# Performance work log

Hardware: AMD Instinct MI355X
Metric: run time of the kernel (lower is better)

The kernel has to match this reference:

```python
import jax, jax.numpy as jnp
import numpy as np
from jax import lax

D_STATE, D_ADAPT, D_CNN, D_RNN, D_OUT, HORIZON = 12, 16, 64, 256, 2, 10
B, L, H, W = 32, 16, 112, 112
DN = ('NCHW', 'OIHW', 'NCHW')
BN_EPS = 1e-5


def setup_inputs() -> dict:
    key = jax.random.key(0)
    ks = jax.random.split(key, 22)
    rn = lambda k, shape, s=0.05: jax.random.normal(k, shape, jnp.float32) * s
    return {
        'x': jax.random.normal(ks[0], (B, L, D_STATE), jnp.float32),
        'frames': jax.random.normal(ks[1], (B, L, 3, H, W), jnp.float32),
        # backbone `cnn`: 16x16 stride-16 patchify conv 3 -> 576 (gives 7x7 spatial)
        'cnn_w': rn(ks[2], (576, 3, 16, 16)), 'cnn_b': rn(ks[3], (576,)),
        # cnn_1: Conv2d(576, 64, 3, padding=1) + ReLU + BatchNorm (eval) + Dropout (eval=identity)
        'cnn1_w': rn(ks[4], (D_CNN, 576, 3, 3)), 'cnn1_b': rn(ks[5], (D_CNN,)),
        'bn_g': jnp.ones((D_CNN,), jnp.float32), 'bn_b': jnp.zeros((D_CNN,), jnp.float32),
        'bn_m': jnp.zeros((D_CNN,), jnp.float32), 'bn_v': jnp.ones((D_CNN,), jnp.float32),
        'a0_w': rn(ks[6], (D_ADAPT, D_STATE)), 'a0_b': rn(ks[7], (D_ADAPT,)),
        'ai_w': rn(ks[8], (D_ADAPT, D_ADAPT)), 'ai_b': rn(ks[9], (D_ADAPT,)),
        'an_w': rn(ks[10], (D_RNN, D_CNN + D_ADAPT)), 'an_b': rn(ks[11], (D_RNN,)),
        # single-layer batch_first GRU, PyTorch gate layout [r, z, n]
        'w_ih': rn(ks[12], (3 * D_RNN, D_RNN)), 'w_hh': rn(ks[13], (3 * D_RNN, D_RNN)),
        'b_ih': rn(ks[14], (3 * D_RNN,)), 'b_hh': rn(ks[15], (3 * D_RNN,)),
        'fi_w': rn(ks[16], (D_RNN, D_RNN)), 'fi_b': rn(ks[17], (D_RNN,)),
        'fn_w': rn(ks[18], (D_OUT, D_RNN)), 'fn_b': rn(ks[19], (D_OUT,)),
    }


def _gru_cell(xt, h, w_ih, w_hh, b_ih, b_hh):
    gi = xt @ w_ih.T + b_ih  # (B, 3*D)
    gh = h @ w_hh.T + b_hh
    i_r, i_z, i_n = jnp.split(gi, 3, axis=-1)
    h_r, h_z, h_n = jnp.split(gh, 3, axis=-1)
    r = jax.nn.sigmoid(i_r + h_r)
    z = jax.nn.sigmoid(i_z + h_z)
    n = jnp.tanh(i_n + r * h_n)
    return (1.0 - z) * n + z * h


def _forward(x, frames, cnn_w, cnn_b, cnn1_w, cnn1_b, bn_g, bn_b, bn_m, bn_v,
             a0_w, a0_b, ai_w, ai_b, an_w, an_b, w_ih, w_hh, b_ih, b_hh,
             fi_w, fi_b, fn_w, fn_b):
    b, l = frames.shape[0], frames.shape[1]
    f = frames.reshape((-1,) + frames.shape[-3:])  # (b*l, 3, H, W)
    # backbone cnn: patchify conv -> (b*l, 576, 7, 7)
    f = lax.conv_general_dilated(f, cnn_w, (16, 16), 'VALID', dimension_numbers=DN) + cnn_b[:, None, None]
    # cnn_1: Conv3x3 same -> ReLU -> BatchNorm(eval) -> Dropout(eval=identity)
    f = lax.conv_general_dilated(f, cnn1_w, (1, 1), 'SAME', dimension_numbers=DN) + cnn1_b[:, None, None]
    f = jax.nn.relu(f)
    inv = bn_g / jnp.sqrt(bn_v + BN_EPS)
    f = (f - bn_m[:, None, None]) * inv[:, None, None] + bn_b[:, None, None]
    # AdaptiveAvgPool2d((1,1)) then reshape to (b, l, d_cnn)
    f = f.mean(axis=(2, 3)).reshape(b, l, -1)
    # state adapters
    s = jax.nn.relu(x @ a0_w.T + a0_b)
    s = s + jax.nn.relu(s @ ai_w.T + ai_b)
    s = jnp.concatenate([s, f], axis=-1)  # (b, l, d_cnn + d_adapt)
    s = jax.nn.relu(s @ an_w.T + an_b)    # (b, l, d_rnn)
    # encoder GRU over the l frames
    d_rnn = w_hh.shape[1]
    h0 = jnp.zeros((b, d_rnn), s.dtype)
    def enc_step(h, xt):
        h2 = _gru_cell(xt, h, w_ih, w_hh, b_ih, b_hh)
        return h2, None
    h, _ = lax.scan(enc_step, h0, jnp.swapaxes(s, 0, 1))
    x_in = h  # last output of single-layer GRU == final hidden state
    def dec_step(carry, _):
        xi, hh = carry
        hn = _gru_cell(xi, hh, w_ih, w_hh, b_ih, b_hh)  # one GRU step; output == new hidden
        xr = hn + jax.nn.relu(hn @ fi_w.T + fi_b)       # final_i residual
        pred = jnp.tanh(xr @ fn_w.T + fn_b)             # final_n head
        return (xr, hn), pred
    _, preds = lax.scan(dec_step, (x_in, h), None, length=HORIZON)
    return preds[:, :, None, :]  # (horizon, b, 1, d_out) matching torch.stack of (b,1,d_out)


def reference(x, frames, cnn_w, cnn_b, cnn1_w, cnn1_b, bn_g, bn_b, bn_m, bn_v,
              a0_w, a0_b, ai_w, ai_b, an_w, an_b, w_ih, w_hh, b_ih, b_hh,
              fi_w, fi_b, fn_w, fn_b):
    return _forward(x, frames, cnn_w, cnn_b, cnn1_w, cnn1_b, bn_g, bn_b, bn_m, bn_v,
                    a0_w, a0_b, ai_w, ai_b, an_w, an_b, w_ih, w_hh, b_ih, b_hh,
                    fi_w, fi_b, fn_w, fn_b)
```

## Files before the change

### kernel.cpp

```cpp
#include <hip/hip_runtime.h>

typedef unsigned short u16;
typedef unsigned int u32;
typedef __bf16 bf16x8 __attribute__((ext_vector_type(8)));
typedef float f32x4 __attribute__((ext_vector_type(4)));
typedef unsigned short u16x8 __attribute__((ext_vector_type(8)));
typedef unsigned int u32x4 __attribute__((ext_vector_type(4)));
typedef _Float16 v2h __attribute__((ext_vector_type(2)));

__device__ __forceinline__ u16 f2bf(float f) {
    unsigned u = __float_as_uint(f);
    u = (u + 0x7fffu + ((u >> 16) & 1u)) >> 16;
    return (u16)u;
}
__device__ __forceinline__ float bf2f(u16 h) {
    return __uint_as_float((unsigned)h << 16);
}
__device__ __forceinline__ u32 packh2(float a, float b) {
    _Float16 ha = (_Float16)a, hb = (_Float16)b;
    u16 la = __builtin_bit_cast(u16, ha), lb = __builtin_bit_cast(u16, hb);
    return (u32)la | ((u32)lb << 16);
}
__device__ __forceinline__ float dot2acc(u32 w, u32 h, float acc) {
#if __has_builtin(__builtin_amdgcn_fdot2)
    return __builtin_amdgcn_fdot2(__builtin_bit_cast(v2h, w),
                                  __builtin_bit_cast(v2h, h), acc, false);
#else
    v2h wv = __builtin_bit_cast(v2h, w), hv = __builtin_bit_cast(v2h, h);
    return acc + (float)wv.x * (float)hv.x + (float)wv.y * (float)hv.y;
#endif
}
__device__ __forceinline__ float dot8(u32x4 w, u32x4 h, float acc) {
    acc = dot2acc(w.x, h.x, acc);
    acc = dot2acc(w.y, h.y, acc);
    acc = dot2acc(w.z, h.z, acc);
    acc = dot2acc(w.w, h.w, acc);
    return acc;
}
__device__ __forceinline__ void gload_lds16(const void* g, void* l) {
    __builtin_amdgcn_global_load_lds(
        (const __attribute__((address_space(1))) unsigned int*)g,
        (__attribute__((address_space(3))) unsigned int*)l, 16, 0, 0);
}
__device__ __forceinline__ void barrier_lds() {
    __builtin_amdgcn_s_waitcnt(0xC07F);
    __builtin_amdgcn_s_barrier();
}

__global__ __launch_bounds__(256) void prep_kernel(
    const float* __restrict__ cnn_w, const float* __restrict__ cnn1_w,
    const float* __restrict__ w_hh, const float* __restrict__ w_ih,
    const float* __restrict__ fi_w, const float* __restrict__ frames,
    u16* __restrict__ B1, u16* __restrict__ B2,
    u32* __restrict__ whh8, u32* __restrict__ wih8, u32* __restrict__ fi8,
    u32* __restrict__ zpage, u16* __restrict__ fbf)
{
    if (blockIdx.x >= 3924) {
        size_t i = ((size_t)(blockIdx.x - 3924) * 256 + threadIdx.x) * 8;
        float4 a = *(const float4*)(frames + i);
        float4 b = *(const float4*)(frames + i + 4);
        u16x8 v = { f2bf(a.x), f2bf(a.y), f2bf(a.z), f2bf(a.w),
                    f2bf(b.x), f2bf(b.y), f2bf(b.z), f2bf(b.w) };
        __builtin_nontemporal_store(v, (u16x8*)(fbf + i));
        return;
    }
    int idx = blockIdx.x * 256 + threadIdx.x;
    if (idx < 442368) { B1[idx] = f2bf(cnn_w[idx]); return; }
    idx -= 442368;
    if (idx < 331776) {
        int n = idx / 5184, rem = idx - n * 5184;
        int off = rem / 576, c = rem - off * 576;
        int dy = off / 3, dx = off - dy * 3;
        B2[idx] = f2bf(cnn1_w[((n * 576 + c) * 3 + dy) * 3 + dx]);
        return;
    }
    idx -= 331776;
    if (idx < 98304) {
        int kb = idx / 3072, r = idx - kb * 3072;
        int o = r >> 2, c = r & 3;
        int kk = kb * 8 + c * 2;
        whh8[idx] = packh2(w_hh[o * 256 + kk], w_hh[o * 256 + kk + 1]);
        return;
    }
    idx -= 98304;
    if (idx < 98304) {
        int kb = idx / 3072, r = idx - kb * 3072;
        int o = r >> 2, c = r & 3;
        int kk = kb * 8 + c * 2;
        wih8[idx] = packh2(w_ih[o * 256 + kk], w_ih[o * 256 + kk + 1]);
        return;
    }
    idx -= 98304;
    if (idx < 32768) {
        int kb = idx / 1024, r = idx - kb * 1024;
        int u = r >> 2, c = r & 3;
        int kk = kb * 8 + c * 2;
        fi8[idx] = packh2(fi_w[u * 256 + kk], fi_w[u * 256 + kk + 1]);
        return;
    }
    idx -= 32768;
    if (idx < 1024) zpage[idx] = 0u;
}

__global__ __launch_bounds__(256) void gemm1_v2(
    const u16* __restrict__ fbf, const u16* __restrict__ B1,
    const float* __restrict__ cnn_b, u16* __restrict__ f1)
{
    __shared__ u16 As[128 * 64];
    __shared__ u16 Bs[64 * 64];
    const int t = threadIdx.x, bx = blockIdx.x;
    const int m0 = (bx / 9) * 128, n0 = (bx % 9) * 64;
    const int wave = t >> 6, lane = t & 63;
    const int lm = lane & 15, lq = lane >> 4;

    f32x4 acc[2][4];
#pragma unroll
    for (int i = 0; i < 2; ++i)
#pragma unroll
        for (int q = 0; q < 4; ++q) acc[i][q] = (f32x4){0.f, 0.f, 0.f, 0.f};

    int ac8[4]; size_t abase[4];
#pragma unroll
    for (int i = 0; i < 4; ++i) {
        int s = wave * 256 + i * 64 + lane;
        int row = s >> 3, cc = s & 7;
        ac8[i] = cc ^ (row & 7);
        int m = m0 + row;
        int fr = m / 49, pos = m - fr * 49;
        int py = pos / 7, px = pos - py * 7;
        abase[i] = (size_t)fr * 37632 + py * 1792 + px * 16;
    }
    int bn[2], bc8[2];
#pragma unroll
    for (int i = 0; i < 2; ++i) {
        int s = wave * 128 + i * 64 + lane;
        int n = s >> 3, cc = s & 7;
        bn[i] = n; bc8[i] = cc ^ (n & 7);
    }

    for (int kt = 0; kt < 12; ++kt) {
        const int k0 = kt * 64;
#pragma unroll
        for (int i = 0; i < 4; ++i) {
            int k = k0 + ac8[i] * 8;
            int c = k >> 8, dy = (k >> 4) & 15, dx = k & 15;
            gload_lds16(fbf + abase[i] + c * 12544 + dy * 112 + dx,
                        &As[(wave * 256 + i * 64) * 8]);
        }
#pragma unroll
        for (int i = 0; i < 2; ++i) {
            gload_lds16(B1 + (size_t)(n0 + bn[i]) * 768 + k0 + bc8[i] * 8,
                        &Bs[(wave * 128 + i * 64) * 8]);
        }
        __syncthreads();
#pragma unroll
        for (int s = 0; s < 2; ++s) {
            bf16x8 a[2], b[4];
#pragma unroll
            for (int mi = 0; mi < 2; ++mi) {
                int row = wave * 32 + mi * 16 + lm;
                int c8 = s * 4 + lq;
                a[mi] = *(const bf16x8*)(&As[(row * 8 + (c8 ^ (row & 7))) * 8]);
            }
#pragma unroll
            for (int q = 0; q < 4; ++q) {
                int n = q * 16 + lm;
                int c8 = s * 4 + lq;
                b[q] = *(const bf16x8*)(&Bs[(n * 8 + (c8 ^ (n & 7))) * 8]);
            }
#pragma unroll
            for (int mi = 0; mi < 2; ++mi)
#pragma unroll
                for (int q = 0; q < 4; ++q)
                    acc[mi][q] = __builtin_amdgcn_mfma_f32_16x16x32_bf16(a[mi], b[q], acc[mi][q], 0, 0, 0);
        }
        __syncthreads();
    }
#pragma unroll
    for (int mi = 0; mi < 2; ++mi) {
#pragma unroll
        for (int q = 0; q < 4; ++q) {
            int n = n0 + q * 16 + lm;
            float bias = cnn_b[n];
#pragma unroll
            for (int r = 0; r < 4; ++r) {
                int m = m0 + wave * 32 + mi * 16 + lq * 4 + r;
                __builtin_nontemporal_store(f2bf(acc[mi][q][r] + bias), &f1[(size_t)m * 576 + n]);
            }
        }
    }
}

__global__ __launch_bounds__(256) void gemm1_patchify(
    const float* __restrict__ frames, const u16* __restrict__ B1,
    const float* __restrict__ cnn_b, u16* __restrict__ f1)
{
    __shared__ u16 As[128 * 64];
    __shared__ u16 Bs[64 * 64];
    const int t = threadIdx.x;
    const int bx = blockIdx.x;
    const int m0 = (bx / 9) * 128;
    const int n0 = (bx % 9) * 64;
    const int wave = t >> 6, lane = t & 63;
    const int lm = lane & 15, lq = lane >> 4;

    f32x4 acc[2][4];
#pragma unroll
    for (int i = 0; i < 2; ++i)
#pragma unroll
        for (int q = 0; q < 4; ++q) acc[i][q] = (f32x4){0.f, 0.f, 0.f, 0.f};

    int arow[4], ac8[4], abase[4];
#pragma unroll
    for (int i = 0; i < 4; ++i) {
        int cid = t + i * 256;
        int row = cid >> 3, c8 = cid & 7;
        int m = m0 + row;
        int fr = m / 49, pos = m - fr * 49;
        int py = pos / 7, px = pos - py * 7;
        arow[i] = row; ac8[i] = c8;
        abase[i] = (fr * 3 * 112 + py * 16) * 112 + px * 16;
    }

    for (int kt = 0; kt < 12; ++kt) {
        const int k0 = kt * 64;
#pragma unroll
        for (int i = 0; i < 4; ++i) {
            int k = k0 + ac8[i] * 8;
            int c = k >> 8, dy = (k >> 4) & 15, dx = k & 15;
            const float* src = frames + abase[i] + (c * 112 + dy) * 112 + dx;
            float4 v0 = *(const float4*)src;
            float4 v1 = *(const float4*)(src + 4);
            u16x8 v = { f2bf(v0.x), f2bf(v0.y), f2bf(v0.z), f2bf(v0.w),
                        f2bf(v1.x), f2bf(v1.y), f2bf(v1.z), f2bf(v1.w) };
            int sidx = arow[i] * 8 + (ac8[i] ^ (arow[i] & 7));
            *(u16x8*)(&As[sidx * 8]) = v;
        }
#pragma unroll
        for (int i = 0; i < 2; ++i) {
            int cid = t + i * 256;
            int n = cid >> 3, c8 = cid & 7;
            u16x8 v = *(const u16x8*)(B1 + (size_t)(n0 + n) * 768 + k0 + c8 * 8);
            int sidx = n * 8 + (c8 ^ (n & 7));
            *(u16x8*)(&Bs[sidx * 8]) = v;
        }
        __syncthreads();
#pragma unroll
        for (int s = 0; s < 2; ++s) {
            bf16x8 a[2], b[4];
#pragma unroll
            for (int mi = 0; mi < 2; ++mi) {
                int row = wave * 32 + mi * 16 + lm;
                int c8 = s * 4 + lq;
                a[mi] = *(const bf16x8*)(&As[(row * 8 + (c8 ^ (row & 7))) * 8]);
            }
#pragma unroll
            for (int q = 0; q < 4; ++q) {
                int n = q * 16 + lm;
                int c8 = s * 4 + lq;
                b[q] = *(const bf16x8*)(&Bs[(n * 8 + (c8 ^ (n & 7))) * 8]);
            }
#pragma unroll
            for (int mi = 0; mi < 2; ++mi)
#pragma unroll
                for (int q = 0; q < 4; ++q)
                    acc[mi][q] = __builtin_amdgcn_mfma_f32_16x16x32_bf16(a[mi], b[q], acc[mi][q], 0, 0, 0);
        }
        __syncthreads();
    }
#pragma unroll
    for (int mi = 0; mi < 2; ++mi) {
#pragma unroll
        for (int q = 0; q < 4; ++q) {
            int n = n0 + q * 16 + lm;
            float bias = cnn_b[n];
#pragma unroll
            for (int r = 0; r < 4; ++r) {
                int m = m0 + wave * 32 + mi * 16 + lq * 4 + r;
                __builtin_nontemporal_store(f2bf(acc[mi][q][r] + bias), &f1[(size_t)m * 576 + n]);
            }
        }
    }
}

__global__ __launch_bounds__(256) void gemm2_v2(
    const u16* __restrict__ f1, const u16* __restrict__ B2,
    const u16* __restrict__ zpage, float* __restrict__ C2)
{
    __shared__ u16 As[64 * 64];
    __shared__ u16 Bs[64 * 64];
    const int t = threadIdx.x;
    const int m0 = blockIdx.x * 64;
    const int wave = t >> 6, lane = t & 63;
    const int lm = lane & 15, lq = lane >> 4;

    f32x4 acc[4];
#pragma unroll
    for (int q = 0; q < 4; ++q) acc[q] = (f32x4){0.f, 0.f, 0.f, 0.f};

    int ac8[2], afr[2], apy[2], apx[2];
#pragma unroll
    for (int i = 0; i < 2; ++i) {
        int s = wave * 128 + i * 64 + lane;
        int row = s >> 3, cc = s & 7;
        ac8[i] = cc ^ (row & 7);
        int m = m0 + row;
        int fr = m / 49, pos = m - fr * 49;
        int py = pos / 7;
        afr[i] = fr; apy[i] = py; apx[i] = pos - py * 7;
    }
    int bn[2], bc8[2];
#pragma unroll
    for (int i = 0; i < 2; ++i) {
        int s = wave * 128 + i * 64 + lane;
        int n = s >> 3, cc = s & 7;
        bn[i] = n; bc8[i] = cc ^ (n & 7);
    }

    for (int kt = 0; kt < 81; ++kt) {
        int off = kt / 9, cb = kt - off * 9;
        int dy = off / 3, dx = off - dy * 3;
        int c0 = cb * 64;
#pragma unroll
        for (int i = 0; i < 2; ++i) {
            int yy = apy[i] + dy - 1, xx = apx[i] + dx - 1;
            const u16* g = ((unsigned)yy < 7u && (unsigned)xx < 7u)
                ? f1 + ((size_t)(afr[i] * 49 + yy * 7 + xx)) * 576 + c0 + ac8[i] * 8
                : zpage;
            gload_lds16(g, &As[(wave * 128 + i * 64) * 8]);
        }
#pragma unroll
        for (int i = 0; i < 2; ++i) {
            gload_lds16(B2 + (size_t)bn[i] * 5184 + kt * 64 + bc8[i] * 8,
                        &Bs[(wave * 128 + i * 64) * 8]);
        }
        __syncthreads();
#pragma unroll
        for (int s = 0; s < 2; ++s) {
            int row = wave * 16 + lm;
            int c8 = s * 4 + lq;
            bf16x8 a = *(const bf16x8*)(&As[(row * 8 + (c8 ^ (row & 7))) * 8]);
            bf16x8 b[4];
#pragma unroll
            for (int q = 0; q < 4; ++q) {
                int n = q * 16 + lm;
                b[q] = *(const bf16x8*)(&Bs[(n * 8 + (c8 ^ (n & 7))) * 8]);
            }
#pragma unroll
            for (int q = 0; q < 4; ++q)
                acc[q] = __builtin_amdgcn_mfma_f32_16x16x32_bf16(a, b[q], acc[q], 0, 0, 0);
        }
        __syncthreads();
    }
#pragma unroll
    for (int q = 0; q < 4; ++q)
#pragma unroll
        for (int r = 0; r < 4; ++r) {
            int m = m0 + wave * 16 + lq * 4 + r;
            int n = q * 16 + lm;
            __builtin_nontemporal_store(acc[q][r], &C2[(size_t)m * 64 + n]);
        }
}

__global__ __launch_bounds__(256) void reduce_kernel(
    const float* __restrict__ C2, const float* __restrict__ cnn1_b,
    const float* __restrict__ bn_g, const float* __restrict__ bn_b,
    const float* __restrict__ bn_m, const float* __restrict__ bn_v,
    float* __restrict__ fmean)
{
    int idx = blockIdx.x * 256 + threadIdx.x;
    int bl = idx >> 6, ch = idx & 63;
    float bias = cnn1_b[ch];
    const float* p = C2 + (size_t)bl * 49 * 64 + ch;
    float s = 0.f;
#pragma unroll
    for (int i = 0; i < 49; ++i) s += fmaxf(p[i * 64] + bias, 0.f);
    float mean = s * (1.f / 49.f);
    float inv = bn_g[ch] * rsqrtf(bn_v[ch] + 1e-5f);
    fmean[idx] = (mean - bn_m[ch]) * inv + bn_b[ch];
}

__global__ __launch_bounds__(256) void adapt_prep2_kernel(
    const float* __restrict__ x, const float* __restrict__ fmean,
    const float* __restrict__ a0_w, const float* __restrict__ a0_b,
    const float* __restrict__ ai_w, const float* __restrict__ ai_b,
    const float* __restrict__ an_w, const float* __restrict__ an_b,
    const float* __restrict__ w_ih,
    u16* __restrict__ zx_hi, u16* __restrict__ zx_lo,
    u16* __restrict__ wih_hi, u16* __restrict__ wih_lo)
{
    const int t = threadIdx.x;
    if (blockIdx.x >= 512) {
        int idx = (blockIdx.x - 512) * 256 + t;
        float v = w_ih[idx];
        u16 hi = f2bf(v);
        wih_hi[idx] = hi;
        wih_lo[idx] = f2bf(v - bf2f(hi));
        return;
    }
    const int bl = blockIdx.x;
    __shared__ float s0[16];
    __shared__ float sf[80];
    if (t < 16) {
        float a = a0_b[t];
        const float* xp = x + bl * 12;
#pragma unroll
        for (int i = 0; i < 12; ++i) a += xp[i] * a0_w[t * 12 + i];
        s0[t] = fmaxf(a, 0.f);
    }
    __syncthreads();
    if (t < 16) {
        float a = ai_b[t];
#pragma unroll
        for (int i = 0; i < 16; ++i) a += s0[i] * ai_w[t * 16 + i];
        sf[t] = s0[t] + fmaxf(a, 0.f);
    } else if (t < 80) {
        sf[t] = fmean[bl * 64 + (t - 16)];
    }
    __syncthreads();
    float a = an_b[t];
#pragma unroll 8
    for (int i = 0; i < 80; ++i) a += sf[i] * an_w[t * 80 + i];
    a = fmaxf(a, 0.f);
    u16 hi = f2bf(a);
    zx_hi[bl * 256 + t] = hi;
    zx_lo[bl * 256 + t] = f2bf(a - bf2f(hi));
}

__global__ __launch_bounds__(256) void gi_kernel(
    const u16* __restrict__ zx_hi, const u16* __restrict__ zx_lo,
    const u16* __restrict__ wih_hi, const u16* __restrict__ wih_lo,
    const float* __restrict__ b_ih, float* __restrict__ gi_pre)
{
    __shared__ u16 Ah[128 * 64], Al[128 * 64];
    __shared__ u16 Bh[64 * 64], Bl[64 * 64];
    const int t = threadIdx.x, bx = blockIdx.x;
    const int m0 = (bx / 12) * 128, n0 = (bx % 12) * 64;
    const int wave = t >> 6, lane = t & 63;
    const int lm = lane & 15, lq = lane >> 4;

    f32x4 acc[2][4];
#pragma unroll
    for (int i = 0; i < 2; ++i)
#pragma unroll
        for (int q = 0; q < 4; ++q) acc[i][q] = (f32x4){0.f, 0.f, 0.f, 0.f};

    for (int kt = 0; kt < 4; ++kt) {
        const int k0 = kt * 64;
#pragma unroll
        for (int i = 0; i < 4; ++i) {
            int cid = t + i * 256;
            int row = cid >> 3, c8 = cid & 7;
            size_t src = (size_t)(m0 + row) * 256 + k0 + c8 * 8;
            int sidx = (row * 8 + (c8 ^ (row & 7))) * 8;
            *(u16x8*)(&Ah[sidx]) = *(const u16x8*)(zx_hi + src);
            *(u16x8*)(&Al[sidx]) = *(const u16x8*)(zx_lo + src);
        }
#pragma unroll
        for (int i = 0; i < 2; ++i) {
            int cid = t + i * 256;
            int n = cid >> 3, c8 = cid & 7;
            size_t src = (size_t)(n0 + n) * 256 + k0 + c8 * 8;
            int sidx = (n * 8 + (c8 ^ (n & 7))) * 8;
            *(u16x8*)(&Bh[sidx]) = *(const u16x8*)(wih_hi + src);
            *(u16x8*)(&Bl[sidx]) = *(const u16x8*)(wih_lo + src);
        }
        __syncthreads();
#pragma unroll
        for (int s = 0; s < 2; ++s) {
            bf16x8 ah[2], al[2], bh[4], blv[4];
#pragma unroll
            for (int mi = 0; mi < 2; ++mi) {
                int row = wave * 32 + mi * 16 + lm;
                int c8 = s * 4 + lq;
                int sidx = (row * 8 + (c8 ^ (row & 7))) * 8;
                ah[mi] = *(const bf16x8*)(&Ah[sidx]);
                al[mi] = *(const bf16x8*)(&Al[sidx]);
            }
#pragma unroll
            for (int q = 0; q < 4; ++q) {
                int n = q * 16 + lm;
                int c8 = s * 4 + lq;
                int sidx = (n * 8 + (c8 ^ (n & 7))) * 8;
                bh[q] = *(const bf16x8*)(&Bh[sidx]);
                blv[q] = *(const bf16x8*)(&Bl[sidx]);
            }
#pragma unroll
            for (int mi = 0; mi < 2; ++mi)
#pragma unroll
                for (int q = 0; q < 4; ++q) {
                    acc[mi][q] = __builtin_amdgcn_mfma_f32_16x16x32_bf16(ah[mi], bh[q], acc[mi][q], 0, 0, 0);
                    acc[mi][q] = __builtin_amdgcn_mfma_f32_16x16x32_bf16(ah[mi], blv[q], acc[mi][q], 0, 0, 0);
                    acc[mi][q] = __builtin_amdgcn_mfma_f32_16x16x32_bf16(al[mi], bh[q], acc[mi][q], 0, 0, 0);
                }
        }
        __syncthreads();
    }
#pragma unroll
    for (int q = 0; q < 4; ++q) {
        int n = n0 + q * 16 + lm;
        float bias = b_ih[n];
#pragma unroll
        for (int mi = 0; mi < 2; ++mi)
#pragma unroll
            for (int r = 0; r < 4; ++r) {
                int m = m0 + wave * 32 + mi * 16 + lq * 4 + r;
                gi_pre[(size_t)m * 768 + n] = acc[mi][q][r] + bias;
            }
    }
}

__global__ __launch_bounds__(768) void rnn_stream5(
    const float* __restrict__ gi_pre,
    const u32x4* __restrict__ whh8, const u32x4* __restrict__ wih8,
    const u32x4* __restrict__ fi8,
    const float* __restrict__ b_ih, const float* __restrict__ b_hh,
    const float* __restrict__ fi_b,
    const float* __restrict__ fn_w, const float* __restrict__ fn_b,
    float* __restrict__ out)
{
    extern __shared__ __align__(16) u32 slab[];
    const int b = blockIdx.x, t = threadIdx.x;
    const int wave = t >> 6;
    __shared__ __align__(16) u32 h2[128];
    __shared__ __align__(16) u32 x2[128];
    __shared__ float sA[768];
    __shared__ float sB[256];
    __shared__ float parts[768];
    __shared__ float pp[8];

#pragma unroll
    for (int j = 0; j < 12; ++j)
        *(u32x4*)&slab[(j * 768 + t) * 4] = whh8[j * 768 + t];

    u32x4 whr[20];
#pragma unroll
    for (int j = 0; j < 20; ++j) whr[j] = whh8[(size_t)(12 + j) * 768 + t];

    const float bhh = b_hh[t];
    const float bih = b_ih[t];
    float hprev = 0.f;
    if (t < 128) h2[t] = 0u;
    __syncthreads();

    for (int l = 0; l < 16; ++l) {
        float gi = gi_pre[(size_t)(b * 16 + l) * 768 + t];
        float a0 = 0.f, a1 = 0.f;
#pragma unroll
        for (int j = 0; j < 12; ++j) {
            u32x4 ws = *(const u32x4*)&slab[(j * 768 + t) * 4];
            u32x4 hh = *(const u32x4*)&h2[j * 4];
            if (j & 1) a1 = dot8(ws, hh, a1); else a0 = dot8(ws, hh, a0);
        }
#pragma unroll
        for (int j = 0; j < 20; ++j) {
            u32x4 hh = *(const u32x4*)&h2[(12 + j) * 4];
            if (j & 1) a1 = dot8(whr[j], hh, a1); else a0 = dot8(whr[j], hh, a0);
        }
        float ah = a0 + a1;
        if (t < 512) sA[t] = gi + ah + bhh;
        else { sA[t] = gi; sB[t - 512] = ah + bhh; }
        barrier_lds();
        if (t < 256) {
            float r = 1.f / (1.f + expf(-sA[t]));
            float z = 1.f / (1.f + expf(-sA[256 + t]));
            float n = tanhf(sA[512 + t] + r * sB[t]);
            hprev = (1.f - z) * n + z * hprev;
            float partner = __shfl_xor(hprev, 1);
            if ((t & 1) == 0) h2[t >> 1] = packh2(hprev, partner);
        }
        barrier_lds();
    }

    float xprev = hprev;
    if (t < 128) x2[t] = h2[t];
    __syncthreads();
    const int u_ = t & 255, s_ = t >> 8;

    for (int d = 0; d < 10; ++d) {
        float a0 = 0.f, a1 = 0.f, x0 = 0.f, x1 = 0.f;
#pragma unroll 4
        for (int j = 0; j < 32; ++j) {
            int jj = (j + wave * 3) & 31;
            u32x4 w = wih8[(size_t)jj * 768 + t];
            u32x4 xx = *(const u32x4*)&x2[jj * 4];
            if (j & 1) x1 = dot8(w, xx, x1); else x0 = dot8(w, xx, x0);
        }
#pragma unroll
        for (int j = 0; j < 12; ++j) {
            u32x4 ws = *(const u32x4*)&slab[(j * 768 + t) * 4];
            u32x4 hh = *(const u32x4*)&h2[j * 4];
            if (j & 1) a1 = dot8(ws, hh, a1); else a0 = dot8(ws, hh, a0);
        }
#pragma unroll
        for (int j = 0; j < 20; ++j) {
            u32x4 hh = *(const u32x4*)&h2[(12 + j) * 4];
            if (j & 1) a1 = dot8(whr[j], hh, a1); else a0 = dot8(whr[j], hh, a0);
        }
        float ah = a0 + a1, ax = x0 + x1;
        if (t < 512) sA[t] = ax + bih + ah + bhh;
        else { sA[t] = ax + bih; sB[t - 512] = ah + bhh; }
        barrier_lds();
        u32x4 fw[11];
        int cnt = 0;
#pragma unroll
        for (int j = 0; j < 11; ++j) {
            int jj = s_ + j * 3;
            if (jj < 32) { fw[j] = fi8[jj * 256 + u_]; cnt = j + 1; }
        }
        if (t < 256) {
            float r = 1.f / (1.f + expf(-sA[t]));
            float z = 1.f / (1.f + expf(-sA[256 + t]));
            float n = tanhf(sA[512 + t] + r * sB[t]);
            hprev = (1.f - z) * n + z * hprev;
            float partner = __shfl_xor(hprev, 1);
            if ((t & 1) == 0) h2[t >> 1] = packh2(hprev, partner);
        }
        barrier_lds();
        {
            float f0 = 0.f, f1v = 0.f;
#pragma unroll
            for (int j = 0; j < 11; ++j) {
                if (j < cnt) {
                    int jj = s_ + j * 3;
                    u32x4 hh = *(const u32x4*)&h2[jj * 4];
                    if (j & 1) f1v = dot8(fw[j], hh, f1v); else f0 = dot8(fw[j], hh, f0);
                }
            }
            parts[t] = f0 + f1v;
        }
        barrier_lds();
        if (t < 256) {
            float a = parts[t] + parts[256 + t] + parts[512 + t] + fi_b[t];
            xprev = hprev + fmaxf(a, 0.f);
            float partner = __shfl_xor(xprev, 1);
            if ((t & 1) == 0) x2[t >> 1] = packh2(xprev, partner);
            float c0 = xprev * fn_w[t];
            float c1 = xprev * fn_w[256 + t];
#pragma unroll
            for (int off = 32; off >= 1; off >>= 1) {
                c0 += __shfl_down(c0, off);
                c1 += __shfl_down(c1, off);
            }
            if ((t & 63) == 0) { pp[(t >> 6) * 2] = c0; pp[(t >> 6) * 2 + 1] = c1; }
        }
        barrier_lds();
        if (t < 2)
            out[d * 64 + b * 2 + t] =
                tanhf(fn_b[t] + pp[t] + pp[2 + t] + pp[4 + t] + pp[6 + t]);
    }
}

extern "C" void kernel_launch(void* const* d_in, const int* in_sizes, int n_in,
                              void* d_out, int out_size, void* d_ws, size_t ws_size,
                              hipStream_t stream)
{
    const float* x      = (const float*)d_in[0];
    const float* frames = (const float*)d_in[1];
    const float* cnn_w  = (const float*)d_in[2];
    const float* cnn_b  = (const float*)d_in[3];
    const float* cnn1_w = (const float*)d_in[4];
    const float* cnn1_b = (const float*)d_in[5];
    const float* bn_g   = (const float*)d_in[6];
    const float* bn_b   = (const float*)d_in[7];
    const float* bn_m   = (const float*)d_in[8];
    const float* bn_v   = (const float*)d_in[9];
    const float* a0_w   = (const float*)d_in[10];
    const float* a0_b   = (const float*)d_in[11];
    const float* ai_w   = (const float*)d_in[12];
    const float* ai_b   = (const float*)d_in[13];
    const float* an_w   = (const float*)d_in[14];
    const float* an_b   = (const float*)d_in[15];
    const float* w_ih   = (const float*)d_in[16];
    const float* w_hh   = (const float*)d_in[17];
    const float* b_ih   = (const float*)d_in[18];
    const float* b_hh   = (const float*)d_in[19];
    const float* fi_w   = (const float*)d_in[20];
    const float* fi_b   = (const float*)d_in[21];
    const float* fn_w   = (const float*)d_in[22];
    const float* fn_b   = (const float*)d_in[23];
    float* out = (float*)d_out;

    char* ws = (char*)d_ws;
    u16*   f1     = (u16*)(ws);
    u16*   B1     = (u16*)(ws + 28901376);
    u16*   B2     = (u16*)(ws + 29786112);
    float* C2     = (float*)(ws + 30449664);
    float* fmean  = (float*)(ws + 36872192);
    u32*   whh8   = (u32*)(ws + 37003264);
    u32*   wih8   = (u32*)(ws + 37396480);
    u32*   fi8    = (u32*)(ws + 37789696);
    u32*   zpage  = (u32*)(ws + 37920768);
    float* gi_pre = (float*)(ws + 30449664);
    u16*   wih_hi = (u16*)(ws + 32022528);
    u16*   wih_lo = (u16*)(ws + 32415744);
    u16*   zx_hi  = (u16*)(ws + 32808960);
    u16*   zx_lo  = (u16*)(ws + 33071104);
    u16*   fbf    = (u16*)(ws + 37924864);

    const bool big = ws_size >= 76460032ull;

    prep_kernel<<<big ? 13332 : 3924, 256, 0, stream>>>(
        cnn_w, cnn1_w, w_hh, w_ih, fi_w, frames,
        B1, B2, whh8, wih8, fi8, zpage, fbf);
    if (big) {
        gemm1_v2<<<196 * 9, 256, 0, stream>>>(fbf, B1, cnn_b, f1);
    } else {
        gemm1_patchify<<<196 * 9, 256, 0, stream>>>(frames, B1, cnn_b, f1);
    }
    gemm2_v2<<<392, 256, 0, stream>>>(f1, B2, (const u16*)zpage, C2);
    reduce_kernel<<<128, 256, 0, stream>>>(C2, cnn1_b, bn_g, bn_b, bn_m, bn_v, fmean);
    adapt_prep2_kernel<<<1280, 256, 0, stream>>>(x, fmean, a0_w, a0_b, ai_w, ai_b,
                                                 an_w, an_b, w_ih,
                                                 zx_hi, zx_lo, wih_hi, wih_lo);
    gi_kernel<<<48, 256, 0, stream>>>(zx_hi, zx_lo, wih_hi, wih_lo, b_ih, gi_pre);
    hipFuncSetAttribute((const void*)rnn_stream5,
                        hipFuncAttributeMaxDynamicSharedMemorySize, 147456);
    rnn_stream5<<<32, 768, 147456, stream>>>(gi_pre, (const u32x4*)whh8,
                                             (const u32x4*)wih8, (const u32x4*)fi8,
                                             b_ih, b_hh, fi_b, fn_w, fn_b, out);
}
```

Measured before the change: 422.7 us.

## Triple-buffer conv GEMM with larger M tile, stream GRU weights, fast activations

The 3x3 conv GEMM now uses 128-row tiles with a three-stage LDS ring. Async global-to-LDS loads for tile kt+2 are issued while tile kt is computed, with one barrier per step, which should hide load latency and reuse the B tile across more rows. The GRU kernel stops holding 20 w_hh blocks in registers and streams them from global/L2 each step with a staggered start per wave, freeing registers at the cost of repeated weight reads. Sigmoid and tanh switch to __expf-based formulas, which are cheaper but less precise.

```diff
diff --git a/kernel.cpp b/kernel.cpp
--- a/kernel.cpp
+++ b/kernel.cpp
@@ -46,6 +46,8 @@
     __builtin_amdgcn_s_waitcnt(0xC07F);
     __builtin_amdgcn_s_barrier();
 }
+__device__ __forceinline__ float fsig(float x) { return 1.f / (1.f + __expf(-x)); }
+__device__ __forceinline__ float ftanh(float x) { return 1.f - 2.f / (1.f + __expf(2.f * x)); }
 
 __global__ __launch_bounds__(256) void prep_kernel(
     const float* __restrict__ cnn_w, const float* __restrict__ cnn1_w,
@@ -283,25 +285,27 @@
     }
 }
 
-__global__ __launch_bounds__(256) void gemm2_v2(
+__global__ __launch_bounds__(256) void gemm2_v3(
     const u16* __restrict__ f1, const u16* __restrict__ B2,
     const u16* __restrict__ zpage, float* __restrict__ C2)
 {
-    __shared__ u16 As[64 * 64];
-    __shared__ u16 Bs[64 * 64];
+    __shared__ u16 As[3][128 * 64];
+    __shared__ u16 Bs[3][64 * 64];
     const int t = threadIdx.x;
-    const int m0 = blockIdx.x * 64;
+    const int m0 = blockIdx.x * 128;
     const int wave = t >> 6, lane = t & 63;
     const int lm = lane & 15, lq = lane >> 4;
 
-    f32x4 acc[4];
-#pragma unroll
-    for (int q = 0; q < 4; ++q) acc[q] = (f32x4){0.f, 0.f, 0.f, 0.f};
-
-    int ac8[2], afr[2], apy[2], apx[2];
-#pragma unroll
-    for (int i = 0; i < 2; ++i) {
-        int s = wave * 128 + i * 64 + lane;
+    f32x4 acc[2][4];
+#pragma unroll
+    for (int i = 0; i < 2; ++i)
+#pragma unroll
+        for (int q = 0; q < 4; ++q) acc[i][q] = (f32x4){0.f, 0.f, 0.f, 0.f};
+
+    int ac8[4], afr[4], apy[4], apx[4];
+#pragma unroll
+    for (int i = 0; i < 4; ++i) {
+        int s = wave * 256 + i * 64 + lane;
         int row = s >> 3, cc = s & 7;
         ac8[i] = cc ^ (row & 7);
         int m = m0 + row;
@@ -317,49 +321,68 @@
         bn[i] = n; bc8[i] = cc ^ (n & 7);
     }
 
-    for (int kt = 0; kt < 81; ++kt) {
+    auto issue = [&](int kt, int buf) {
         int off = kt / 9, cb = kt - off * 9;
         int dy = off / 3, dx = off - dy * 3;
         int c0 = cb * 64;
 #pragma unroll
-        for (int i = 0; i < 2; ++i) {
+        for (int i = 0; i < 4; ++i) {
             int yy = apy[i] + dy - 1, xx = apx[i] + dx - 1;
             const u16* g = ((unsigned)yy < 7u && (unsigned)xx < 7u)
                 ? f1 + ((size_t)(afr[i] * 49 + yy * 7 + xx)) * 576 + c0 + ac8[i] * 8
                 : zpage;
-            gload_lds16(g, &As[(wave * 128 + i * 64) * 8]);
+            gload_lds16(g, &As[buf][(wave * 256 + i * 64) * 8]);
         }
 #pragma unroll
         for (int i = 0; i < 2; ++i) {
             gload_lds16(B2 + (size_t)bn[i] * 5184 + kt * 64 + bc8[i] * 8,
-                        &Bs[(wave * 128 + i * 64) * 8]);
-        }
-        __syncthreads();
+                        &Bs[buf][(wave * 128 + i * 64) * 8]);
+        }
+    };
+
+    issue(0, 0);
+    issue(1, 1);
+
+    for (int kt = 0; kt < 81; ++kt) {
+        const int cur = kt % 3;
+        if (kt < 80) __builtin_amdgcn_s_waitcnt(0x0F76);
+        else         __builtin_amdgcn_s_waitcnt(0x0F70);
+        __builtin_amdgcn_s_barrier();
+        __asm__ volatile("" ::: "memory");
+        if (kt + 2 <= 80) issue(kt + 2, (kt + 2) % 3);
 #pragma unroll
         for (int s = 0; s < 2; ++s) {
-            int row = wave * 16 + lm;
-            int c8 = s * 4 + lq;
-            bf16x8 a = *(const bf16x8*)(&As[(row * 8 + (c8 ^ (row & 7))) * 8]);
-            bf16x8 b[4];
+            bf16x8 a[2], b[4];
+#pragma unroll
+            for (int mi = 0; mi < 2; ++mi) {
+                int row = wave * 32 + mi * 16 + lm;
+                int c8 = s * 4 + lq;
+                a[mi] = *(const bf16x8*)(&As[cur][(row * 8 + (c8 ^ (row & 7))) * 8]);
+            }
 #pragma unroll
             for (int q = 0; q < 4; ++q) {
                 int n = q * 16 + lm;
-                b[q] = *(const bf16x8*)(&Bs[(n * 8 + (c8 ^ (n & 7))) * 8]);
-            }
-#pragma unroll
-            for (int q = 0; q < 4; ++q)
-                acc[q] = __builtin_amdgcn_mfma_f32_16x16x32_bf16(a, b[q], acc[q], 0, 0, 0);
-        }
-        __syncthreads();
-    }
-#pragma unroll
-    for (int q = 0; q < 4; ++q)
-#pragma unroll
-        for (int r = 0; r < 4; ++r) {
-            int m = m0 + wave * 16 + lq * 4 + r;
-            int n = q * 16 + lm;
-            __builtin_nontemporal_store(acc[q][r], &C2[(size_t)m * 64 + n]);
-        }
+                int c8 = s * 4 + lq;
+                b[q] = *(const bf16x8*)(&Bs[cur][(n * 8 + (c8 ^ (n & 7))) * 8]);
+            }
+#pragma unroll
+            for (int mi = 0; mi < 2; ++mi)
+#pragma unroll
+                for (int q = 0; q < 4; ++q)
+                    acc[mi][q] = __builtin_amdgcn_mfma_f32_16x16x32_bf16(a[mi], b[q], acc[mi][q], 0, 0, 0);
+        }
+        __asm__ volatile("" ::: "memory");
+    }
+#pragma unroll
+    for (int mi = 0; mi < 2; ++mi)
+#pragma unroll
+        for (int q = 0; q < 4; ++q)
+#pragma unroll
+            for (int r = 0; r < 4; ++r) {
+                int m = m0 + wave * 32 + mi * 16 + lq * 4 + r;
+                int n = q * 16 + lm;
+                __builtin_nontemporal_store(acc[mi][q][r], &C2[(size_t)m * 64 + n]);
+            }
 }
 
 __global__ __launch_bounds__(256) void reduce_kernel(
@@ -510,7 +533,7 @@
     }
 }
 
-__global__ __launch_bounds__(768) void rnn_stream5(
+__global__ __launch_bounds__(768) void rnn_stream6(
     const float* __restrict__ gi_pre,
     const u32x4* __restrict__ whh8, const u32x4* __restrict__ wih8,
     const u32x4* __restrict__ fi8,
@@ -533,10 +556,6 @@
     for (int j = 0; j < 12; ++j)
         *(u32x4*)&slab[(j * 768 + t) * 4] = whh8[j * 768 + t];
 
-    u32x4 whr[20];
-#pragma unroll
-    for (int j = 0; j < 20; ++j) whr[j] = whh8[(size_t)(12 + j) * 768 + t];
-
     const float bhh = b_hh[t];
     const float bih = b_ih[t];
     float hprev = 0.f;
@@ -546,25 +565,28 @@
     for (int l = 0; l < 16; ++l) {
         float gi = gi_pre[(size_t)(b * 16 + l) * 768 + t];
         float a0 = 0.f, a1 = 0.f;
+#pragma unroll 4
+        for (int j = 0; j < 20; ++j) {
+            int jj = j + wave; if (jj >= 20) jj -= 20;
+            int kb = 12 + jj;
+            u32x4 w = whh8[(size_t)kb * 768 + t];
+            u32x4 hh = *(const u32x4*)&h2[kb * 4];
+            if (j & 1) a1 = dot8(w, hh, a1); else a0 = dot8(w, hh, a0);
+        }
 #pragma unroll
         for (int j = 0; j < 12; ++j) {
             u32x4 ws = *(const u32x4*)&slab[(j * 768 + t) * 4];
             u32x4 hh = *(const u32x4*)&h2[j * 4];
             if (j & 1) a1 = dot8(ws, hh, a1); else a0 = dot8(ws, hh, a0);
-        }
-#pragma unroll
-        for (int j = 0; j < 20; ++j) {
-            u32x4 hh = *(const u32x4*)&h2[(12 + j) * 4];
-            if (j & 1) a1 = dot8(whr[j], hh, a1); else a0 = dot8(whr[j], hh, a0);
         }
         float ah = a0 + a1;
         if (t < 512) sA[t] = gi + ah + bhh;
         else { sA[t] = gi; sB[t - 512] = ah + bhh; }
         barrier_lds();
         if (t < 256) {
-            float r = 1.f / (1.f + expf(-sA[t]));
-            float z = 1.f / (1.f + expf(-sA[256 + t]));
-            float n = tanhf(sA[512 + t] + r * sB[t]);
+            float r = fsig(sA[t]);
+            float z = fsig(sA[256 + t]);
+            float n = ftanh(sA[512 + t] + r * sB[t]);
             hprev = (1.f - z) * n + z * hprev;
             float partner = __shfl_xor(hprev, 1);
             if ((t & 1) == 0) h2[t >> 1] = packh2(hprev, partner);
@@ -586,16 +608,19 @@
             u32x4 xx = *(const u32x4*)&x2[jj * 4];
             if (j & 1) x1 = dot8(w, xx, x1); else x0 = dot8(w, xx, x0);
         }
+#pragma unroll 4
+        for (int j = 0; j < 20; ++j) {
+            int jj = j + wave; if (jj >= 20) jj -= 20;
+            int kb = 12 + jj;
+            u32x4 w = whh8[(size_t)kb * 768 + t];
+            u32x4 hh = *(const u32x4*)&h2[kb * 4];
+            if (j & 1) a1 = dot8(w, hh, a1); else a0 = dot8(w, hh, a0);
+        }
 #pragma unroll
         for (int j = 0; j < 12; ++j) {
             u32x4 ws = *(const u32x4*)&slab[(j * 768 + t) * 4];
             u32x4 hh = *(const u32x4*)&h2[j * 4];
             if (j & 1) a1 = dot8(ws, hh, a1); else a0 = dot8(ws, hh, a0);
-        }
-#pragma unroll
-        for (int j = 0; j < 20; ++j) {
-            u32x4 hh = *(const u32x4*)&h2[(12 + j) * 4];
-            if (j & 1) a1 = dot8(whr[j], hh, a1); else a0 = dot8(whr[j], hh, a0);
         }
         float ah = a0 + a1, ax = x0 + x1;
         if (t < 512) sA[t] = ax + bih + ah + bhh;
@@ -609,9 +634,9 @@
             if (jj < 32) { fw[j] = fi8[jj * 256 + u_]; cnt = j + 1; }
         }
         if (t < 256) {
-            float r = 1.f / (1.f + expf(-sA[t]));
-            float z = 1.f / (1.f + expf(-sA[256 + t]));
-            float n = tanhf(sA[512 + t] + r * sB[t]);
+            float r = fsig(sA[t]);
+            float z = fsig(sA[256 + t]);
+            float n = ftanh(sA[512 + t] + r * sB[t]);
             hprev = (1.f - z) * n + z * hprev;
             float partner = __shfl_xor(hprev, 1);
             if ((t & 1) == 0) h2[t >> 1] = packh2(hprev, partner);
@@ -708,15 +733,15 @@
     } else {
         gemm1_patchify<<<196 * 9, 256, 0, stream>>>(frames, B1, cnn_b, f1);
     }
-    gemm2_v2<<<392, 256, 0, stream>>>(f1, B2, (const u16*)zpage, C2);
+    gemm2_v3<<<196, 256, 0, stream>>>(f1, B2, (const u16*)zpage, C2);
     reduce_kernel<<<128, 256, 0, stream>>>(C2, cnn1_b, bn_g, bn_b, bn_m, bn_v, fmean);
     adapt_prep2_kernel<<<1280, 256, 0, stream>>>(x, fmean, a0_w, a0_b, ai_w, ai_b,
                                                  an_w, an_b, w_ih,
                                                  zx_hi, zx_lo, wih_hi, wih_lo);
     gi_kernel<<<48, 256, 0, stream>>>(zx_hi, zx_lo, wih_hi, wih_lo, b_ih, gi_pre);
-    hipFuncSetAttribute((const void*)rnn_stream5,
+    hipFuncSetAttribute((const void*)rnn_stream6,
                         hipFuncAttributeMaxDynamicSharedMemorySize, 147456);
-    rnn_stream5<<<32, 768, 147456, stream>>>(gi_pre, (const u32x4*)whh8,
+    rnn_stream6<<<32, 768, 147456, stream>>>(gi_pre, (const u32x4*)whh8,
                                              (const u32x4*)wih8, (const u32x4*)fi8,
                                              b_ih, b_hh, fi_b, fn_w, fn_b, out);
 }
```

Result: slower. 450.9 us (+6.7%).
